# Kernel optimization log

Hardware: AMD Instinct MI355X
Metric: run time of the kernel (lower is better)

Reference implementation:

```python
import jax, jax.numpy as jnp
import numpy as np

N_NODES = 100000
N_EDGES = 3200000
N_GRAPHS = 512
D_FEAT = 128


def spmm(edge_index, edge_weight, h, n_nodes):
    # out_i = sum_{(i,j) in E} w_ij * h_j   (row = edge_index[0], col = edge_index[1])
    row, col = edge_index[0], edge_index[1]
    msgs = edge_weight[:, None] * h[col]            # [E, F]
    return jax.ops.segment_sum(msgs, row, num_segments=n_nodes)


def gcn_conv(x, edge_index, edge_weight, W, b):
    h = x @ W                                       # project first (Spektral order)
    h = spmm(edge_index, edge_weight, h, x.shape[0]) + b
    return jax.nn.elu(h)


def setup_inputs() -> dict:
    key = jax.random.key(0)
    ks = jax.random.split(key, 12)
    x = jax.random.normal(ks[0], (N_NODES, D_FEAT), dtype=jnp.float32)
    edge_index = jax.random.randint(ks[1], (2, N_EDGES), 0, N_NODES, dtype=jnp.int32)
    edge_weight = jax.random.uniform(ks[2], (N_EDGES,), dtype=jnp.float32)
    seg_ids = jnp.sort(jax.random.randint(ks[3], (N_NODES,), 0, N_GRAPHS, dtype=jnp.int32))
    s = 0.1
    return {
        "x": x,
        "edge_index": edge_index,
        "edge_weight": edge_weight,
        "seg_ids": seg_ids,
        "W1": jax.random.normal(ks[4], (D_FEAT, 32), dtype=jnp.float32) * s,
        "b1": jnp.zeros((32,), jnp.float32),
        "W2": jax.random.normal(ks[5], (32, 32), dtype=jnp.float32) * s,
        "b2": jnp.zeros((32,), jnp.float32),
        "W3": jax.random.normal(ks[6], (32, 32), dtype=jnp.float32) * s,
        "b3": jnp.zeros((32,), jnp.float32),
        "Wd1": jax.random.normal(ks[7], (32, 64), dtype=jnp.float32) * s,
        "bd1": jnp.zeros((64,), jnp.float32),
        "Wd2": jax.random.normal(ks[8], (64, 32), dtype=jnp.float32) * s,
        "bd2": jnp.zeros((32,), jnp.float32),
        "Wd3": jax.random.normal(ks[9], (32, 1), dtype=jnp.float32) * s,
        "bd3": jnp.zeros((1,), jnp.float32),
    }


def reference(x, edge_index, edge_weight, seg_ids, W1, b1, W2, b2, W3, b3,
              Wd1, bd1, Wd2, bd2, Wd3, bd3):
    h = gcn_conv(x, edge_index, edge_weight, W1, b1)
    h = gcn_conv(h, edge_index, edge_weight, W2, b2)
    h = gcn_conv(h, edge_index, edge_weight, W3, b3)
    # GlobalSumPool over graph index (disjoint mode)
    g = jax.ops.segment_sum(h, seg_ids, num_segments=N_GRAPHS)  # [G, 32]
    g = jax.nn.relu(g @ Wd1 + bd1)   # dropout = identity at inference
    g = jax.nn.relu(g @ Wd2 + bd2)
    out = jax.nn.sigmoid(g @ Wd3 + bd3)  # [G, 1]
    return out
```

## Files before the change

kernel.cpp:

```cpp
#include <hip/hip_runtime.h>
#include <hip/hip_fp16.h>
#include <math.h>

#define N_NODES 100000
#define N_EDGES 3200000
#define N_GRAPHS 512
#define D_FEAT 128
#define F_HID 32

#define RPB 128
#define NB 782
#define CAP 5120
#define CHUNK 8192
#define SBS 1024
#define NCHUNK ((N_EDGES + CHUNK - 1) / CHUNK)
#define CTILES 16
#define NKEYS (RPB * CTILES)
#define SPB 64
#define PHASES 8

static __device__ __forceinline__ __half2 u2h2(unsigned u) {
    return *reinterpret_cast<__half2*>(&u);
}

__global__ void gemm128x32(const float* __restrict__ x, const float* __restrict__ W,
                           unsigned short* __restrict__ outh, int n_nodes) {
    __shared__ float Ws[128 * 32];
    for (int i = threadIdx.x; i < 128 * 32; i += 256) Ws[i] = W[i];
    __syncthreads();
    const int fg = threadIdx.x & 7;
    const int nl = threadIdx.x >> 3;
    const int node = blockIdx.x * 32 + nl;
    if (node >= n_nodes) return;
    const float4* x4 = (const float4*)(x + (size_t)node * 128);
    const float4* Ws4 = (const float4*)Ws;
    float4 acc = make_float4(0.f, 0.f, 0.f, 0.f);
    for (int kk = 0; kk < 32; ++kk) {
        float4 xv = x4[kk];
        int k = kk * 4;
        float4 w0 = Ws4[(k + 0) * 8 + fg];
        float4 w1 = Ws4[(k + 1) * 8 + fg];
        float4 w2 = Ws4[(k + 2) * 8 + fg];
        float4 w3 = Ws4[(k + 3) * 8 + fg];
        acc.x += xv.x * w0.x + xv.y * w1.x + xv.z * w2.x + xv.w * w3.x;
        acc.y += xv.x * w0.y + xv.y * w1.y + xv.z * w2.y + xv.w * w3.y;
        acc.z += xv.x * w0.z + xv.y * w1.z + xv.z * w2.z + xv.w * w3.z;
        acc.w += xv.x * w0.w + xv.y * w1.w + xv.z * w2.w + xv.w * w3.w;
    }
    __half2 p0 = __floats2half2_rn(acc.x, acc.y);
    __half2 p1 = __floats2half2_rn(acc.z, acc.w);
    uint2 o = make_uint2(*reinterpret_cast<unsigned*>(&p0),
                         *reinterpret_cast<unsigned*>(&p1));
    ((uint2*)(outh + (size_t)node * 32))[fg] = o;
}

__global__ void init_cursor(int* __restrict__ cursor) {
    int t = blockIdx.x * blockDim.x + threadIdx.x;
    if (t < NB) cursor[t] = t * CAP;
}

__global__ __launch_bounds__(SBS) void bucket_scatter(
        const int* __restrict__ row, const int* __restrict__ col,
        const float* __restrict__ w, int* __restrict__ cursor,
        uint2* __restrict__ rec, int n_edges) {
    __shared__ uint2 srt[CHUNK];
    __shared__ int hist[NB];
    __shared__ int lofs[NB + 1];
    __shared__ int lbase[NB];
    __shared__ int tsum[SBS];
    __shared__ unsigned short flr[CHUNK / 16];
    const int t = threadIdx.x;
    const int base = blockIdx.x * CHUNK;
    const int count = min(CHUNK, n_edges - base);

    if (t < NB) hist[t] = 0;
    __syncthreads();
    int rloc[CHUNK / SBS];
    #pragma unroll
    for (int j = 0; j < CHUNK / SBS; ++j) {
        int i = t + j * SBS;
        int r = -1;
        if (i < count) { r = row[base + i]; atomicAdd(&hist[r >> 7], 1); }
        rloc[j] = r;
    }
    __syncthreads();
    int v = (t < NB) ? hist[t] : 0;
    tsum[t] = v;
    __syncthreads();
    for (int off = 1; off < SBS; off <<= 1) {
        int add = (t >= off) ? tsum[t - off] : 0;
        __syncthreads();
        tsum[t] += add;
        __syncthreads();
    }
    if (t < NB) lofs[t] = tsum[t] - v;
    if (t == SBS - 1) lofs[NB] = tsum[SBS - 1];
    __syncthreads();
    if (t < NB) {
        lbase[t] = v ? atomicAdd(&cursor[t], v) : 0;
        hist[t] = 0;
    }
    for (int q = t; q < CHUNK / 16; q += SBS) {
        int pos = q * 16;
        int lo = 0, hi = NB;
        while (hi - lo > 1) {
            int mid = (lo + hi) >> 1;
            if (lofs[mid] <= pos) lo = mid; else hi = mid;
        }
        flr[q] = (unsigned short)lo;
    }
    __syncthreads();
    #pragma unroll
    for (int j = 0; j < CHUNK / SBS; ++j) {
        int i = t + j * SBS;
        if (i < count) {
            int e = base + i;
            int r = rloc[j];
            int b = r >> 7;
            int pos = lofs[b] + atomicAdd(&hist[b], 1);
            srt[pos] = make_uint2(((unsigned)(r & 127) << 17) | (unsigned)col[e],
                                  __float_as_uint(w[e]));
        }
    }
    __syncthreads();
    for (int i = t; i < count; i += SBS) {
        uint2 vv = srt[i];
        int b = flr[i >> 4];
        while (lofs[b + 1] <= i) ++b;
        rec[lbase[b] + (i - lofs[b])] = vv;
    }
}

__global__ void scan_nb(const int* __restrict__ cursor, int* __restrict__ bbase) {
    __shared__ int s[1024];
    const int t = threadIdx.x;
    int v = (t < NB) ? (cursor[t] - t * CAP) : 0;
    s[t] = v;
    __syncthreads();
    for (int off = 1; off < 1024; off <<= 1) {
        int add = (t >= off) ? s[t - off] : 0;
        __syncthreads();
        s[t] += add;
        __syncthreads();
    }
    if (t < NB) bbase[t] = s[t] - v;
    if (t == NB - 1) bbase[NB] = s[t];
}

__global__ __launch_bounds__(512) void bucket_sort(
        const int* __restrict__ cursor, const int* __restrict__ bbase,
        const uint2* __restrict__ rec, unsigned* __restrict__ rec2,
        int* __restrict__ row_ptr, int n_nodes) {
    __shared__ unsigned srt[CAP];
    __shared__ int hist[NKEYS];
    __shared__ int lofs[NKEYS];
    __shared__ int tsum[512];
    const int t = threadIdx.x;
    const int b = blockIdx.x;
    const int sbase = b * CAP;
    const int cnt = cursor[b] - sbase;
    const int gbase = bbase[b];

    for (int i = t; i < NKEYS; i += 512) hist[i] = 0;
    __syncthreads();
    for (int i = t; i < cnt; i += 512) {
        unsigned rx = rec[sbase + i].x;
        int key = (rx >> 17) * CTILES + ((rx & 0x1FFFFu) >> 13);
        atomicAdd(&hist[key], 1);
    }
    __syncthreads();
    int vals[4];
    int s0 = 0;
    const int k4 = t * 4;
    #pragma unroll
    for (int j = 0; j < 4; ++j) { vals[j] = hist[k4 + j]; s0 += vals[j]; }
    tsum[t] = s0;
    __syncthreads();
    for (int off = 1; off < 512; off <<= 1) {
        int add = (t >= off) ? tsum[t - off] : 0;
        __syncthreads();
        tsum[t] += add;
        __syncthreads();
    }
    {
        int run = tsum[t] - s0;
        #pragma unroll
        for (int j = 0; j < 4; ++j) { lofs[k4 + j] = run; run += vals[j]; }
    }
    __syncthreads();
    if (t < RPB) {
        int gr = b * RPB + t;
        if (gr <= n_nodes) row_ptr[gr] = gbase + lofs[t * CTILES];
    }
    for (int i = t; i < NKEYS; i += 512) hist[i] = lofs[i];
    __syncthreads();
    for (int i = t; i < cnt; i += 512) {
        uint2 v = rec[sbase + i];
        int key = (v.x >> 17) * CTILES + ((v.x & 0x1FFFFu) >> 13);
        int pos = atomicAdd(&hist[key], 1);
        float wf = __uint_as_float(v.y);
        __half hw = __float2half_rn(wf);
        unsigned wb = ((unsigned)*reinterpret_cast<unsigned short*>(&hw)) & 0x7FFFu;
        srt[pos] = (wb << 17) | (v.x & 0x1FFFFu);
    }
    __syncthreads();
    for (int i = t; i < cnt; i += 512)
        rec2[gbase + i] = srt[i];
}

#define CONSUME(G, P) do {                                          \
    unsigned wu_ = (P) >> 17; wu_ |= wu_ << 16;                     \
    __half2 w2_ = u2h2(wu_);                                        \
    a0 = __hfma2(w2_, u2h2((G).x), a0);                             \
    a1 = __hfma2(w2_, u2h2((G).y), a1);                             \
    a2 = __hfma2(w2_, u2h2((G).z), a2);                             \
    a3 = __hfma2(w2_, u2h2((G).w), a3); } while (0)

#define EDGE1 do {                                                  \
    unsigned p0_ = rec2[i];                                         \
    uint4 g0_ = h4[(size_t)(p0_ & 0x1FFFF) * 4 + fl];               \
    CONSUME(g0_, p0_); } while (0)

__global__ __launch_bounds__(256) void spmm_fused(
        const int* __restrict__ rp, const unsigned* __restrict__ rec2,
        const unsigned short* __restrict__ h_in, const float* __restrict__ bias,
        const float* __restrict__ Wn,
        unsigned short* __restrict__ h_out,
        const int* __restrict__ seg,
        float* __restrict__ G,
        int n_nodes) {
    __shared__ float Ws[32 * 32];
    __shared__ float vt[SPB][33];
    const int t = threadIdx.x;
    if (Wn) for (int i = t; i < 1024; i += 256) Ws[i] = Wn[i];
    const int fl = t & 3;
    const int nl = t >> 2;
    const int node = blockIdx.x * SPB + nl;
    const bool valid = node < n_nodes;
    const int s = valid ? rp[node] : 0;
    const int e = valid ? rp[node + 1] : 0;
    const int d = e - s;
    const uint4* h4 = (const uint4*)h_in;
    __half2 a0 = u2h2(0), a1 = u2h2(0), a2 = u2h2(0), a3 = u2h2(0);
    int i = s;
    #pragma unroll
    for (int ph = 1; ph <= PHASES; ++ph) {
        const int end = s + (d * ph) / PHASES;
        for (; i + 4 <= end; i += 4) {
            unsigned p0 = rec2[i];
            unsigned p1 = rec2[i + 1];
            unsigned p2 = rec2[i + 2];
            unsigned p3 = rec2[i + 3];
            uint4 g0 = h4[(size_t)(p0 & 0x1FFFF) * 4 + fl];
            uint4 g1 = h4[(size_t)(p1 & 0x1FFFF) * 4 + fl];
            uint4 g2 = h4[(size_t)(p2 & 0x1FFFF) * 4 + fl];
            uint4 g3 = h4[(size_t)(p3 & 0x1FFFF) * 4 + fl];
            CONSUME(g0, p0); CONSUME(g1, p1);
            CONSUME(g2, p2); CONSUME(g3, p3);
        }
        for (; i < end; ++i) EDGE1;
    }

    float acc[8];
    acc[0] = __low2float(a0); acc[1] = __high2float(a0);
    acc[2] = __low2float(a1); acc[3] = __high2float(a1);
    acc[4] = __low2float(a2); acc[5] = __high2float(a2);
    acc[6] = __low2float(a3); acc[7] = __high2float(a3);
    float4 bv0 = ((const float4*)bias)[fl * 2];
    float4 bv1 = ((const float4*)bias)[fl * 2 + 1];
    acc[0] += bv0.x; acc[1] += bv0.y; acc[2] += bv0.z; acc[3] += bv0.w;
    acc[4] += bv1.x; acc[5] += bv1.y; acc[6] += bv1.z; acc[7] += bv1.w;
    #pragma unroll
    for (int j = 0; j < 8; ++j)
        acc[j] = acc[j] > 0.f ? acc[j] : (expf(acc[j]) - 1.f);
    {
        float* vr = &vt[nl][fl * 8];
        #pragma unroll
        for (int j = 0; j < 8; ++j) vr[j] = acc[j];
    }
    __syncthreads();

    if (Wn) {
        const float4* Ws4 = (const float4*)Ws;
        const float* vrow = vt[nl];
        float o[8] = {0.f, 0.f, 0.f, 0.f, 0.f, 0.f, 0.f, 0.f};
        #pragma unroll 8
        for (int k = 0; k < 32; ++k) {
            float vk = vrow[k];
            float4 w0 = Ws4[k * 8 + fl * 2];
            float4 w1 = Ws4[k * 8 + fl * 2 + 1];
            o[0] += vk * w0.x; o[1] += vk * w0.y; o[2] += vk * w0.z; o[3] += vk * w0.w;
            o[4] += vk * w1.x; o[5] += vk * w1.y; o[6] += vk * w1.z; o[7] += vk * w1.w;
        }
        if (valid) {
            __half2 q0 = __floats2half2_rn(o[0], o[1]);
            __half2 q1 = __floats2half2_rn(o[2], o[3]);
            __half2 q2 = __floats2half2_rn(o[4], o[5]);
            __half2 q3 = __floats2half2_rn(o[6], o[7]);
            uint4 ob = make_uint4(*reinterpret_cast<unsigned*>(&q0),
                                  *reinterpret_cast<unsigned*>(&q1),
                                  *reinterpret_cast<unsigned*>(&q2),
                                  *reinterpret_cast<unsigned*>(&q3));
            ((uint4*)h_out)[(size_t)node * 4 + fl] = ob;
        }
    } else {
        const int f = t & 31;
        const int sub = t >> 5;
        float run = 0.f;
        int cur = -1;
        #pragma unroll
        for (int q = 0; q < 8; ++q) {
            int nloc = sub * 8 + q;
            int node2 = blockIdx.x * SPB + nloc;
            if (node2 >= n_nodes) break;
            int sg = seg[node2];
            if (sg != cur) {
                if (cur >= 0) atomicAdd(&G[(size_t)cur * 32 + f], run);
                cur = sg;
                run = 0.f;
            }
            run += vt[nloc][f];
        }
        if (cur >= 0) atomicAdd(&G[(size_t)cur * 32 + f], run);
    }
}

__global__ void head_mlp(const float* __restrict__ g,
                         const float* __restrict__ Wd1, const float* __restrict__ bd1,
                         const float* __restrict__ Wd2, const float* __restrict__ bd2,
                         const float* __restrict__ Wd3, const float* __restrict__ bd3,
                         float* __restrict__ out) {
    __shared__ float gr[32];
    __shared__ float s1[64];
    __shared__ float s2[32];
    const int gid = blockIdx.x;
    const int t = threadIdx.x;
    if (t < 32) gr[t] = g[(size_t)gid * 32 + t];
    __syncthreads();
    float a = bd1[t];
    for (int k = 0; k < 32; ++k) a += gr[k] * Wd1[k * 64 + t];
    s1[t] = fmaxf(a, 0.f);
    __syncthreads();
    if (t < 32) {
        float a2 = bd2[t];
        for (int k = 0; k < 64; ++k) a2 += s1[k] * Wd2[k * 32 + t];
        s2[t] = fmaxf(a2, 0.f);
    }
    __syncthreads();
    if (t == 0) {
        float a3 = bd3[0];
        for (int k = 0; k < 32; ++k) a3 += s2[k] * Wd3[k];
        out[gid] = 1.f / (1.f + expf(-a3));
    }
}

extern "C" void kernel_launch(void* const* d_in, const int* in_sizes, int n_in,
                              void* d_out, int out_size, void* d_ws, size_t ws_size,
                              hipStream_t stream) {
    const float* x   = (const float*)d_in[0];
    const int*   ei  = (const int*)d_in[1];
    const float* ew  = (const float*)d_in[2];
    const int*   seg = (const int*)d_in[3];
    const float* W1  = (const float*)d_in[4];
    const float* b1  = (const float*)d_in[5];
    const float* W2  = (const float*)d_in[6];
    const float* b2  = (const float*)d_in[7];
    const float* W3  = (const float*)d_in[8];
    const float* b3  = (const float*)d_in[9];
    const float* Wd1 = (const float*)d_in[10];
    const float* bd1 = (const float*)d_in[11];
    const float* Wd2 = (const float*)d_in[12];
    const float* bd2 = (const float*)d_in[13];
    const float* Wd3 = (const float*)d_in[14];
    const float* bd3 = (const float*)d_in[15];
    float* out = (float*)d_out;

    const int* rowp = ei;
    const int* colp = ei + N_EDGES;

    const size_t NF  = (size_t)N_NODES * F_HID;
    const size_t REC_BYTES = (size_t)NB * CAP * sizeof(uint2);

    char*  wsb     = (char*)d_ws;
    uint2* rec     = (uint2*)wsb;
    unsigned short* hA = (unsigned short*)wsb;
    unsigned short* hB = (unsigned short*)(wsb + NF * 2);
    unsigned* rec2 = (unsigned*)(wsb + REC_BYTES);
    int*   cursor  = (int*)(rec2 + N_EDGES);
    int*   bbase   = cursor + NB;
    int*   row_ptr = bbase + NB + 1;
    float* G       = (float*)(row_ptr + N_NODES + 1);

    const int gemm_grid = (N_NODES + 31) / 32;
    const int spmm_grid = (N_NODES + SPB - 1) / SPB;

    init_cursor<<<(NB + 255) / 256, 256, 0, stream>>>(cursor);
    bucket_scatter<<<NCHUNK, SBS, 0, stream>>>(rowp, colp, ew, cursor, rec, N_EDGES);
    scan_nb<<<1, 1024, 0, stream>>>(cursor, bbase);
    bucket_sort<<<NB, 512, 0, stream>>>(cursor, bbase, rec, rec2, row_ptr, N_NODES);
    hipMemsetAsync(G, 0, (size_t)N_GRAPHS * F_HID * sizeof(float), stream);

    gemm128x32<<<gemm_grid, 256, 0, stream>>>(x, W1, hA, N_NODES);
    spmm_fused<<<spmm_grid, 256, 0, stream>>>(row_ptr, rec2, hA, b1, W2, hB, nullptr, nullptr, N_NODES);

    spmm_fused<<<spmm_grid, 256, 0, stream>>>(row_ptr, rec2, hB, b2, W3, hA, nullptr, nullptr, N_NODES);

    spmm_fused<<<spmm_grid, 256, 0, stream>>>(row_ptr, rec2, hA, b3, nullptr, nullptr, seg, G, N_NODES);

    head_mlp<<<N_GRAPHS, 64, 0, stream>>>(G, Wd1, bd1, Wd2, bd2, Wd3, bd3, out);
}
```

Before: 182.5 us.

## Process two node rows per thread with column-range phased sweeps in SpMM

Each SpMM block now handles two 64-node tiles (block b and b+782), halving the grid to 782 blocks. Edge sweeps advance in 13 phases keyed on actual column-index thresholds (8192-wide column ranges, since edges are sorted by column tile) instead of fractional degree splits. The aim is to keep all threads gathering from the same region of h at the same time for L2 locality, and to give each thread two independent gather streams for more memory-level parallelism. The cost is extra branching per sweep, a second epilogue with an added barrier, and fewer resident blocks.

```diff
diff --git a/kernel.cpp b/kernel.cpp
--- a/kernel.cpp
+++ b/kernel.cpp
@@ -17,7 +17,8 @@
 #define CTILES 16
 #define NKEYS (RPB * CTILES)
 #define SPB 64
-#define PHASES 8
+#define PBLK 782
+#define PH 13
 
 static __device__ __forceinline__ __half2 u2h2(unsigned u) {
     return *reinterpret_cast<__half2*>(&u);
@@ -208,18 +209,104 @@
         rec2[gbase + i] = srt[i];
 }
 
-#define CONSUME(G, P) do {                                          \
+#define CONS(b0, b1, b2, b3, G, P) do {                             \
     unsigned wu_ = (P) >> 17; wu_ |= wu_ << 16;                     \
     __half2 w2_ = u2h2(wu_);                                        \
-    a0 = __hfma2(w2_, u2h2((G).x), a0);                             \
-    a1 = __hfma2(w2_, u2h2((G).y), a1);                             \
-    a2 = __hfma2(w2_, u2h2((G).z), a2);                             \
-    a3 = __hfma2(w2_, u2h2((G).w), a3); } while (0)
-
-#define EDGE1 do {                                                  \
-    unsigned p0_ = rec2[i];                                         \
-    uint4 g0_ = h4[(size_t)(p0_ & 0x1FFFF) * 4 + fl];               \
-    CONSUME(g0_, p0_); } while (0)
+    b0 = __hfma2(w2_, u2h2((G).x), b0);                             \
+    b1 = __hfma2(w2_, u2h2((G).y), b1);                             \
+    b2 = __hfma2(w2_, u2h2((G).z), b2);                             \
+    b3 = __hfma2(w2_, u2h2((G).w), b3); } while (0)
+
+#define SWEEP(I, E, b0, b1, b2, b3, THR) do {                       \
+    while (I < E) {                                                 \
+        if (I + 4 <= E) {                                           \
+            unsigned q0 = rec2[I],     q1 = rec2[I + 1],            \
+                     q2 = rec2[I + 2], q3 = rec2[I + 3];            \
+            if ((q3 & 0x1FFFFu) < (THR)) {                          \
+                uint4 g0 = h4[(size_t)(q0 & 0x1FFFF) * 4 + fl];     \
+                uint4 g1 = h4[(size_t)(q1 & 0x1FFFF) * 4 + fl];     \
+                uint4 g2 = h4[(size_t)(q2 & 0x1FFFF) * 4 + fl];     \
+                uint4 g3 = h4[(size_t)(q3 & 0x1FFFF) * 4 + fl];     \
+                CONS(b0, b1, b2, b3, g0, q0);                       \
+                CONS(b0, b1, b2, b3, g1, q1);                       \
+                CONS(b0, b1, b2, b3, g2, q2);                       \
+                CONS(b0, b1, b2, b3, g3, q3);                       \
+                I += 4; continue;                                   \
+            }                                                       \
+        }                                                           \
+        unsigned q_ = rec2[I];                                      \
+        if ((q_ & 0x1FFFFu) >= (THR)) break;                        \
+        uint4 g_ = h4[(size_t)(q_ & 0x1FFFF) * 4 + fl];             \
+        CONS(b0, b1, b2, b3, g_, q_);                               \
+        ++I;                                                        \
+    }                                                               \
+} while (0)
+
+#define EPILOG(NODE, VALID, b0, b1, b2, b3, CBLK) do {              \
+    float acc[8];                                                   \
+    acc[0] = __low2float(b0); acc[1] = __high2float(b0);            \
+    acc[2] = __low2float(b1); acc[3] = __high2float(b1);            \
+    acc[4] = __low2float(b2); acc[5] = __high2float(b2);            \
+    acc[6] = __low2float(b3); acc[7] = __high2float(b3);            \
+    float4 bv0 = ((const float4*)bias)[fl * 2];                     \
+    float4 bv1 = ((const float4*)bias)[fl * 2 + 1];                 \
+    acc[0] += bv0.x; acc[1] += bv0.y; acc[2] += bv0.z; acc[3] += bv0.w; \
+    acc[4] += bv1.x; acc[5] += bv1.y; acc[6] += bv1.z; acc[7] += bv1.w; \
+    _Pragma("unroll")                                               \
+    for (int j = 0; j < 8; ++j)                                     \
+        acc[j] = acc[j] > 0.f ? acc[j] : (expf(acc[j]) - 1.f);      \
+    {                                                               \
+        float* vr = &vt[nl][fl * 8];                                \
+        _Pragma("unroll")                                           \
+        for (int j = 0; j < 8; ++j) vr[j] = acc[j];                 \
+    }                                                               \
+    __syncthreads();                                                \
+    if (Wn) {                                                       \
+        const float4* Ws4 = (const float4*)Ws;                      \
+        const float* vrow = vt[nl];                                 \
+        float o[8] = {0.f, 0.f, 0.f, 0.f, 0.f, 0.f, 0.f, 0.f};      \
+        _Pragma("unroll 8")                                         \
+        for (int k = 0; k < 32; ++k) {                              \
+            float vk = vrow[k];                                     \
+            float4 w0 = Ws4[k * 8 + fl * 2];                        \
+            float4 w1 = Ws4[k * 8 + fl * 2 + 1];                    \
+            o[0] += vk * w0.x; o[1] += vk * w0.y;                   \
+            o[2] += vk * w0.z; o[3] += vk * w0.w;                   \
+            o[4] += vk * w1.x; o[5] += vk * w1.y;                   \
+            o[6] += vk * w1.z; o[7] += vk * w1.w;                   \
+        }                                                           \
+        if (VALID) {                                                \
+            __half2 q0 = __floats2half2_rn(o[0], o[1]);             \
+            __half2 q1 = __floats2half2_rn(o[2], o[3]);             \
+            __half2 q2 = __floats2half2_rn(o[4], o[5]);             \
+            __half2 q3 = __floats2half2_rn(o[6], o[7]);             \
+            uint4 ob = make_uint4(*reinterpret_cast<unsigned*>(&q0),\
+                                  *reinterpret_cast<unsigned*>(&q1),\
+                                  *reinterpret_cast<unsigned*>(&q2),\
+                                  *reinterpret_cast<unsigned*>(&q3));\
+            ((uint4*)h_out)[(size_t)(NODE) * 4 + fl] = ob;          \
+        }                                                           \
+    } else {                                                        \
+        const int f = t & 31;                                       \
+        const int sub = t >> 5;                                     \
+        float run = 0.f;                                            \
+        int cur = -1;                                               \
+        _Pragma("unroll")                                           \
+        for (int q = 0; q < 8; ++q) {                               \
+            int nloc = sub * 8 + q;                                 \
+            int node2 = (CBLK) * SPB + nloc;                        \
+            if (node2 >= n_nodes) break;                            \
+            int sg = seg[node2];                                    \
+            if (sg != cur) {                                        \
+                if (cur >= 0) atomicAdd(&G[(size_t)cur * 32 + f], run); \
+                cur = sg;                                           \
+                run = 0.f;                                          \
+            }                                                       \
+            run += vt[nloc][f];                                     \
+        }                                                           \
+        if (cur >= 0) atomicAdd(&G[(size_t)cur * 32 + f], run);     \
+    }                                                               \
+} while (0)
 
 __global__ __launch_bounds__(256) void spmm_fused(
         const int* __restrict__ rp, const unsigned* __restrict__ rec2,
@@ -235,94 +322,25 @@
     if (Wn) for (int i = t; i < 1024; i += 256) Ws[i] = Wn[i];
     const int fl = t & 3;
     const int nl = t >> 2;
-    const int node = blockIdx.x * SPB + nl;
-    const bool valid = node < n_nodes;
-    const int s = valid ? rp[node] : 0;
-    const int e = valid ? rp[node + 1] : 0;
-    const int d = e - s;
+    const int nodeA = blockIdx.x * SPB + nl;
+    const int nodeB = (blockIdx.x + PBLK) * SPB + nl;
+    const bool vA = nodeA < n_nodes;
+    const bool vB = nodeB < n_nodes;
+    int sA = 0, eA = 0, sB = 0, eB = 0;
+    if (vA) { sA = rp[nodeA]; eA = rp[nodeA + 1]; }
+    if (vB) { sB = rp[nodeB]; eB = rp[nodeB + 1]; }
     const uint4* h4 = (const uint4*)h_in;
-    __half2 a0 = u2h2(0), a1 = u2h2(0), a2 = u2h2(0), a3 = u2h2(0);
-    int i = s;
-    #pragma unroll
-    for (int ph = 1; ph <= PHASES; ++ph) {
-        const int end = s + (d * ph) / PHASES;
-        for (; i + 4 <= end; i += 4) {
-            unsigned p0 = rec2[i];
-            unsigned p1 = rec2[i + 1];
-            unsigned p2 = rec2[i + 2];
-            unsigned p3 = rec2[i + 3];
-            uint4 g0 = h4[(size_t)(p0 & 0x1FFFF) * 4 + fl];
-            uint4 g1 = h4[(size_t)(p1 & 0x1FFFF) * 4 + fl];
-            uint4 g2 = h4[(size_t)(p2 & 0x1FFFF) * 4 + fl];
-            uint4 g3 = h4[(size_t)(p3 & 0x1FFFF) * 4 + fl];
-            CONSUME(g0, p0); CONSUME(g1, p1);
-            CONSUME(g2, p2); CONSUME(g3, p3);
-        }
-        for (; i < end; ++i) EDGE1;
-    }
-
-    float acc[8];
-    acc[0] = __low2float(a0); acc[1] = __high2float(a0);
-    acc[2] = __low2float(a1); acc[3] = __high2float(a1);
-    acc[4] = __low2float(a2); acc[5] = __high2float(a2);
-    acc[6] = __low2float(a3); acc[7] = __high2float(a3);
-    float4 bv0 = ((const float4*)bias)[fl * 2];
-    float4 bv1 = ((const float4*)bias)[fl * 2 + 1];
-    acc[0] += bv0.x; acc[1] += bv0.y; acc[2] += bv0.z; acc[3] += bv0.w;
-    acc[4] += bv1.x; acc[5] += bv1.y; acc[6] += bv1.z; acc[7] += bv1.w;
-    #pragma unroll
-    for (int j = 0; j < 8; ++j)
-        acc[j] = acc[j] > 0.f ? acc[j] : (expf(acc[j]) - 1.f);
-    {
-        float* vr = &vt[nl][fl * 8];
-        #pragma unroll
-        for (int j = 0; j < 8; ++j) vr[j] = acc[j];
-    }
-    __syncthreads();
-
-    if (Wn) {
-        const float4* Ws4 = (const float4*)Ws;
-        const float* vrow = vt[nl];
-        float o[8] = {0.f, 0.f, 0.f, 0.f, 0.f, 0.f, 0.f, 0.f};
-        #pragma unroll 8
-        for (int k = 0; k < 32; ++k) {
-            float vk = vrow[k];
-            float4 w0 = Ws4[k * 8 + fl * 2];
-            float4 w1 = Ws4[k * 8 + fl * 2 + 1];
-            o[0] += vk * w0.x; o[1] += vk * w0.y; o[2] += vk * w0.z; o[3] += vk * w0.w;
-            o[4] += vk * w1.x; o[5] += vk * w1.y; o[6] += vk * w1.z; o[7] += vk * w1.w;
-        }
-        if (valid) {
-            __half2 q0 = __floats2half2_rn(o[0], o[1]);
-            __half2 q1 = __floats2half2_rn(o[2], o[3]);
-            __half2 q2 = __floats2half2_rn(o[4], o[5]);
-            __half2 q3 = __floats2half2_rn(o[6], o[7]);
-            uint4 ob = make_uint4(*reinterpret_cast<unsigned*>(&q0),
-                                  *reinterpret_cast<unsigned*>(&q1),
-                                  *reinterpret_cast<unsigned*>(&q2),
-                                  *reinterpret_cast<unsigned*>(&q3));
-            ((uint4*)h_out)[(size_t)node * 4 + fl] = ob;
-        }
-    } else {
-        const int f = t & 31;
-        const int sub = t >> 5;
-        float run = 0.f;
-        int cur = -1;
-        #pragma unroll
-        for (int q = 0; q < 8; ++q) {
-            int nloc = sub * 8 + q;
-            int node2 = blockIdx.x * SPB + nloc;
-            if (node2 >= n_nodes) break;
-            int sg = seg[node2];
-            if (sg != cur) {
-                if (cur >= 0) atomicAdd(&G[(size_t)cur * 32 + f], run);
-                cur = sg;
-                run = 0.f;
-            }
-            run += vt[nloc][f];
-        }
-        if (cur >= 0) atomicAdd(&G[(size_t)cur * 32 + f], run);
-    }
+    __half2 A0 = u2h2(0), A1 = u2h2(0), A2 = u2h2(0), A3 = u2h2(0);
+    __half2 B0 = u2h2(0), B1 = u2h2(0), B2 = u2h2(0), B3 = u2h2(0);
+    int iA = sA, iB = sB;
+    for (int ph = 1; ph <= PH; ++ph) {
+        const unsigned thr = (unsigned)ph << 13;
+        SWEEP(iA, eA, A0, A1, A2, A3, thr);
+        SWEEP(iB, eB, B0, B1, B2, B3, thr);
+    }
+    EPILOG(nodeA, vA, A0, A1, A2, A3, blockIdx.x);
+    __syncthreads();
+    EPILOG(nodeB, vB, B0, B1, B2, B3, blockIdx.x + PBLK);
 }
 
 __global__ void head_mlp(const float* __restrict__ g,
@@ -392,7 +410,6 @@
     float* G       = (float*)(row_ptr + N_NODES + 1);
 
     const int gemm_grid = (N_NODES + 31) / 32;
-    const int spmm_grid = (N_NODES + SPB - 1) / SPB;
 
     init_cursor<<<(NB + 255) / 256, 256, 0, stream>>>(cursor);
     bucket_scatter<<<NCHUNK, SBS, 0, stream>>>(rowp, colp, ew, cursor, rec, N_EDGES);
@@ -401,11 +418,11 @@
     hipMemsetAsync(G, 0, (size_t)N_GRAPHS * F_HID * sizeof(float), stream);
 
     gemm128x32<<<gemm_grid, 256, 0, stream>>>(x, W1, hA, N_NODES);
-    spmm_fused<<<spmm_grid, 256, 0, stream>>>(row_ptr, rec2, hA, b1, W2, hB, nullptr, nullptr, N_NODES);
-
-    spmm_fused<<<spmm_grid, 256, 0, stream>>>(row_ptr, rec2, hB, b2, W3, hA, nullptr, nullptr, N_NODES);
-
-    spmm_fused<<<spmm_grid, 256, 0, stream>>>(row_ptr, rec2, hA, b3, nullptr, nullptr, seg, G, N_NODES);
+    spmm_fused<<<PBLK, 256, 0, stream>>>(row_ptr, rec2, hA, b1, W2, hB, nullptr, nullptr, N_NODES);
+
+    spmm_fused<<<PBLK, 256, 0, stream>>>(row_ptr, rec2, hB, b2, W3, hA, nullptr, nullptr, N_NODES);
+
+    spmm_fused<<<PBLK, 256, 0, stream>>>(row_ptr, rec2, hA, b3, nullptr, nullptr, seg, G, N_NODES);
 
     head_mlp<<<N_GRAPHS, 64, 0, stream>>>(G, Wd1, bd1, Wd2, bd2, Wd3, bd3, out);
 }
```

Result: slower. 354.3 us (+94.2%).
